# Kernel tuning notes

Measured on AMD Instinct MI355X. Metric: run time of the kernel, lower is better.

Reference implementation:

```python
import jax, jax.numpy as jnp
import numpy as np
from jax import lax

B, N = 4, 32768          # clouds, points per cloud (offsets are equal-sized)
CIN, COUT, S = 128, 256, 2048  # in_channels, out_channels, num_samples
EPS = 1e-5               # BatchNorm eps


def fps(xyz, npoint=S):
    """Farthest point sampling over xyz [N,3]; deterministic start index 0.
    Mirrors the torch loop: record current farthest, update min-distance, argmax."""
    n = xyz.shape[0]

    def step(carry, _):
        distance, farthest = carry
        centroid = xyz[farthest]                       # [3]
        dist = jnp.sum((xyz - centroid) ** 2, axis=1)  # [N]
        distance = jnp.minimum(distance, dist)
        new_farthest = jnp.argmax(distance).astype(jnp.int32)
        return (distance, new_farthest), farthest

    init = (jnp.full((n,), 1e10, dtype=xyz.dtype), jnp.int32(0))
    _, centroids = lax.scan(step, init, None, length=npoint)
    return centroids  # [npoint] int32


def setup_inputs():
    key = jax.random.key(0)
    k1, k2, k3 = jax.random.split(key, 3)
    coord = jax.random.normal(k1, (B * N, 3), dtype=jnp.float32)
    feat = jax.random.normal(k2, (B * N, CIN), dtype=jnp.float32)
    offset = (jnp.arange(1, B + 1, dtype=jnp.int32)) * N  # cumulative counts
    W = jax.random.normal(k3, (COUT, CIN), dtype=jnp.float32) / np.sqrt(CIN)
    gamma = jnp.ones((COUT,), dtype=jnp.float32)
    beta = jnp.zeros((COUT,), dtype=jnp.float32)
    return {"coord": coord, "feat": feat, "offset": offset,
            "W": W, "gamma": gamma, "beta": beta}


def reference(coord, feat, offset, W, gamma, beta):
    # fc -> PointBatchNorm (training-mode batch stats over B*N rows) -> ReLU
    x = feat @ W.T                                  # [B*N, COUT]
    mean = jnp.mean(x, axis=0)
    var = jnp.mean((x - mean) ** 2, axis=0)         # biased var, as torch BN
    x = (x - mean) * lax.rsqrt(var + EPS) * gamma + beta
    x = jax.nn.relu(x)

    coord_b = coord.reshape(B, N, 3)
    feat_b = x.reshape(B, N, COUT)
    idx = jax.vmap(fps)(coord_b)                    # [B, S] int32

    new_coords = jnp.take_along_axis(coord_b, idx[..., None], axis=1).reshape(B * S, 3)
    new_feats = jnp.take_along_axis(feat_b, idx[..., None], axis=1).reshape(B * S, COUT)
    new_offsets = jnp.arange(1, B + 1, dtype=jnp.int32) * S
    return new_coords, new_feats, new_offsets
```

## Files before the change

### kernel.cpp

```cpp
#include <hip/hip_runtime.h>

#define NB 4
#define NPT 32768
#define HPT 16384
#define CIN 128
#define COUT 256
#define NS 2048
#define THR 512
#define PPT 32
#define NG 8

#define WS_G 0
#define WS_FSUM 16384
#define WS_SLOT 16512
#define WS_GSCALE 16544
#define WS_GBIAS 16800
#define WS_IDX 17056

#define OUT_COORD 0
#define OUT_FEAT 24576
#define OUT_OFFS 2121728

__global__ __launch_bounds__(THR) void fused1(
    const float* __restrict__ coord, const float* __restrict__ feat,
    float* __restrict__ wsf, int* __restrict__ wsi,
    unsigned long long* __restrict__ slots)
{
  __shared__ float4 ldsd[NG][THR];
  __shared__ int s_widx[2];
  __shared__ int s_gmaxb[2];
  __shared__ int s_bcast;
  __shared__ float s_fs[4][128];

  const int bid = blockIdx.x;
  const int t = threadIdx.x;
  const bool is_fps = (bid < 4) || (bid >= 8 && bid < 12);

  if (is_fps) {
    const int cl = bid & 3;
    const int h = bid >> 3;
    const int gbase = h * HPT;
    const float* xyz = coord + (size_t)cl * NPT * 3;
    int* idx_out = wsi + cl * NS;
    unsigned long long* slot = slots + cl * 4;

    float px[PPT], py[PPT], pz[PPT];
#pragma unroll
    for (int j = 0; j < PPT; ++j) {
      int p = gbase + j * THR + t;
      px[j] = xyz[p * 3 + 0];
      py[j] = xyz[p * 3 + 1];
      pz[j] = xyz[p * 3 + 2];
    }
#pragma unroll
    for (int g = 0; g < NG; ++g)
      ldsd[g][t] = make_float4(1e10f, 1e10f, 1e10f, 1e10f);
    if (t == 0) {
      if (h == 0) idx_out[0] = 0;
      s_widx[0] = s_widx[1] = 0x7fffffff;
      s_gmaxb[0] = s_gmaxb[1] = 0;
    }
    float cx = xyz[0], cy = xyz[1], cz = xyz[2];
    __syncthreads();

    const int lane = t & 63;
    for (int it = 1; it < NS; ++it) {
      const int par = it & 1;
      float mxa = -1.f, mxb = -1.f;
#pragma unroll
      for (int g = 0; g < NG; ++g) {
        float4 d = ldsd[g][t];
        float nd[4];
#pragma unroll
        for (int k = 0; k < 4; ++k) {
          const int j = 4 * g + k;
          float dx = px[j] - cx, dy = py[j] - cy, dz = pz[j] - cz;
          float sx = dx * dx, sy = dy * dy, sz = dz * dz;
          asm volatile("" : "+v"(sx), "+v"(sy), "+v"(sz));
          float dist = (sx + sy) + sz;
          nd[k] = fminf(k == 0 ? d.x : k == 1 ? d.y : k == 2 ? d.z : d.w, dist);
        }
        ldsd[g][t] = make_float4(nd[0], nd[1], nd[2], nd[3]);
        mxa = fmaxf(mxa, fmaxf(nd[0], nd[1]));
        mxb = fmaxf(mxb, fmaxf(nd[2], nd[3]));
      }
      float lmax = fmaxf(mxa, mxb);
      float wm = lmax;
#pragma unroll
      for (int o = 32; o > 0; o >>= 1) wm = fmaxf(wm, __shfl_xor(wm, o, 64));
      if (lane == 0) atomicMax(&s_gmaxb[par], __float_as_int(wm));
      __syncthreads();
      if (t == 0) { s_gmaxb[par ^ 1] = 0; s_widx[par ^ 1] = 0x7fffffff; }
      const float gmax = __int_as_float(s_gmaxb[par]);
      if (lmax == gmax) {
        int best = 0x7fffffff;
#pragma unroll
        for (int g = 0; g < NG; ++g) {
          float4 d = ldsd[g][t];
          if (d.x == gmax) best = min(best, gbase + (4 * g + 0) * THR + t);
          if (d.y == gmax) best = min(best, gbase + (4 * g + 1) * THR + t);
          if (d.z == gmax) best = min(best, gbase + (4 * g + 2) * THR + t);
          if (d.w == gmax) best = min(best, gbase + (4 * g + 3) * THR + t);
        }
        atomicMin(&s_widx[par], best);
      }
      __syncthreads();
      if (t == 0) {
        unsigned long long mine =
            ((unsigned long long)it << 48) |
            ((unsigned long long)(unsigned)s_gmaxb[par] << 15) |
            (unsigned)(32767 - s_widx[par]);
        __hip_atomic_store(&slot[h * 2 + par], mine,
                           __ATOMIC_RELAXED, __HIP_MEMORY_SCOPE_AGENT);
        unsigned long long other;
        do {
          other = __hip_atomic_load(&slot[(1 - h) * 2 + par],
                                    __ATOMIC_RELAXED, __HIP_MEMORY_SCOPE_AGENT);
        } while ((other >> 48) != (unsigned long long)it);
        unsigned long long win = mine > other ? mine : other;
        int widx = 32767 - (int)(win & 0x7fff);
        s_bcast = widx;
        if (h == 0) idx_out[it] = widx;
      }
      __syncthreads();
      const int widx = s_bcast;
      cx = xyz[widx * 3 + 0];
      cy = xyz[widx * 3 + 1];
      cz = xyz[widx * 3 + 2];
    }
  } else {
    const int g = (bid < 8) ? (bid - 4) : (bid - 8);
    if (g < 128) {
      const float* fr = feat + (size_t)g * 1024 * CIN;
      const int ti = (t & 31) * 4;
      const int tj = (t >> 5) * 8;
      float acc[4][8];
#pragma unroll
      for (int a = 0; a < 4; ++a)
#pragma unroll
        for (int b2 = 0; b2 < 8; ++b2) acc[a][b2] = 0.f;
#pragma unroll 4
      for (int r = 0; r < 1024; ++r) {
        const float* rowp = fr + r * CIN;
        float4 a4 = *(const float4*)(rowp + ti);
        float4 b4 = *(const float4*)(rowp + tj);
        float4 b5 = *(const float4*)(rowp + tj + 4);
        float av[4] = {a4.x, a4.y, a4.z, a4.w};
        float bv[8] = {b4.x, b4.y, b4.z, b4.w, b5.x, b5.y, b5.z, b5.w};
#pragma unroll
        for (int a = 0; a < 4; ++a)
#pragma unroll
          for (int b2 = 0; b2 < 8; ++b2) acc[a][b2] += av[a] * bv[b2];
      }
      float* G = wsf + WS_G;
#pragma unroll
      for (int a = 0; a < 4; ++a)
#pragma unroll
        for (int b2 = 0; b2 < 8; ++b2)
          atomicAdd(&G[(ti + a) * CIN + (tj + b2)], acc[a][b2]);
    } else {
      const int fb = g - 128;
      const size_t base = (size_t)fb * 16384;
      const int c = t & 127, rg = t >> 7;
      float s = 0.f;
      for (int r = rg; r < 16384; r += 4)
        s += feat[(base + r) * CIN + c];
      s_fs[rg][c] = s;
      __syncthreads();
      if (t < 128) {
        float v = s_fs[0][t] + s_fs[1][t] + s_fs[2][t] + s_fs[3][t];
        atomicAdd(&wsf[WS_FSUM + t], v);
      }
    }
  }
}

__global__ __launch_bounds__(128) void finalize_k(
    const float* __restrict__ W, const float* __restrict__ gamma,
    const float* __restrict__ beta, float* __restrict__ wsf)
{
  const int c = blockIdx.x, i = threadIdx.x;
  const float* G = wsf + WS_G;
  const float* fsum = wsf + WS_FSUM;
  const float* Gi = G + i * CIN;
  const float* Wc = W + c * CIN;
  float td = 0.f;
#pragma unroll 8
  for (int j = 0; j < CIN; j += 4) {
    float4 g4 = *(const float4*)(Gi + j);
    float4 w4 = *(const float4*)(Wc + j);
    td += g4.x * w4.x + g4.y * w4.y + g4.z * w4.z + g4.w * w4.w;
  }
  const float wci = Wc[i];
  float q = wci * td;
  float m = fsum[i] * wci;
#pragma unroll
  for (int o = 32; o > 0; o >>= 1) {
    q += __shfl_xor(q, o, 64);
    m += __shfl_xor(m, o, 64);
  }
  __shared__ float sq[2], sm[2];
  if ((i & 63) == 0) { sq[i >> 6] = q; sm[i >> 6] = m; }
  __syncthreads();
  if (i == 0) {
    const float inv_m = 1.f / 131072.f;
    float mean = (sm[0] + sm[1]) * inv_m;
    float e2 = (sq[0] + sq[1]) * inv_m;
    float var = e2 - mean * mean;
    float rstd = rsqrtf(var + 1e-5f);
    float gs = gamma[c] * rstd;
    wsf[WS_GSCALE + c] = gs;
    wsf[WS_GBIAS + c] = beta[c] - mean * gs;
  }
}

__global__ __launch_bounds__(256) void gather_k(
    const float* __restrict__ coord, const float* __restrict__ feat,
    const float* __restrict__ W, const float* __restrict__ wsf,
    const int* __restrict__ wsi, float* __restrict__ out)
{
  const int p = blockIdx.x, t = threadIdx.x;
  const int b = p >> 11;
  const int idx = wsi[p];
  const size_t row = (size_t)b * NPT + idx;
  __shared__ float lf[CIN];
  if (t < CIN) lf[t] = feat[row * CIN + t];
  __syncthreads();
  const float* Wc = W + t * CIN;
  float acc = 0.f;
#pragma unroll 8
  for (int k = 0; k < CIN; k += 4) {
    float4 w4 = *(const float4*)(Wc + k);
    acc += lf[k] * w4.x + lf[k + 1] * w4.y + lf[k + 2] * w4.z + lf[k + 3] * w4.w;
  }
  float y = fmaxf(fmaf(acc, wsf[WS_GSCALE + t], wsf[WS_GBIAS + t]), 0.f);
  out[OUT_FEAT + (size_t)p * COUT + t] = y;
  if (t < 3) out[OUT_COORD + p * 3 + t] = coord[row * 3 + t];
  if (p == 0 && t < 4) out[OUT_OFFS + t] = (float)((t + 1) * NS);
}

extern "C" void kernel_launch(void* const* d_in, const int* in_sizes, int n_in,
                              void* d_out, int out_size, void* d_ws, size_t ws_size,
                              hipStream_t stream)
{
  const float* coord = (const float*)d_in[0];
  const float* feat  = (const float*)d_in[1];
  const float* W     = (const float*)d_in[3];
  const float* gamma = (const float*)d_in[4];
  const float* beta  = (const float*)d_in[5];
  float* wsf = (float*)d_ws;
  int* wsi = (int*)(wsf + WS_IDX);
  unsigned long long* slots = (unsigned long long*)(wsf + WS_SLOT);
  float* out = (float*)d_out;

  hipMemsetAsync(d_ws, 0, (WS_SLOT + 32) * sizeof(float), stream);

  fused1<<<144, THR, 0, stream>>>(coord, feat, wsf, wsi, slots);
  finalize_k<<<COUT, 128, 0, stream>>>(W, gamma, beta, wsf);
  gather_k<<<NB * NS, 256, 0, stream>>>(coord, feat, W, wsf, wsi, out);
}
```

Measured before the change: 5.331 ms.

## Split each FPS cloud across four blocks with register distances and packed argmax keys

Each point cloud's farthest-point sampling now runs on four cooperating blocks instead of two, so each thread holds 16 points. The running min-distances stay in registers rather than in LDS. The two-phase max-then-index reduction is replaced by one 64-bit packed (distance, index) key reduced with shuffles and one LDS atomicMax, which removes a barrier and the rescan. The cross-block handshake now polls three peer slots per iteration, which may add global-memory polling latency on the serial 2048-step critical path.

```diff
diff --git a/kernel.cpp b/kernel.cpp
--- a/kernel.cpp
+++ b/kernel.cpp
@@ -2,20 +2,19 @@
 
 #define NB 4
 #define NPT 32768
-#define HPT 16384
+#define QPT 8192
 #define CIN 128
 #define COUT 256
 #define NS 2048
 #define THR 512
-#define PPT 32
-#define NG 8
+#define PPT 16
 
 #define WS_G 0
 #define WS_FSUM 16384
 #define WS_SLOT 16512
-#define WS_GSCALE 16544
-#define WS_GBIAS 16800
-#define WS_IDX 17056
+#define WS_GSCALE 16576
+#define WS_GBIAS 16832
+#define WS_IDX 17088
 
 #define OUT_COORD 0
 #define OUT_FEAT 24576
@@ -26,39 +25,34 @@
     float* __restrict__ wsf, int* __restrict__ wsi,
     unsigned long long* __restrict__ slots)
 {
-  __shared__ float4 ldsd[NG][THR];
-  __shared__ int s_widx[2];
-  __shared__ int s_gmaxb[2];
+  __shared__ unsigned long long s_key[2];
   __shared__ int s_bcast;
   __shared__ float s_fs[4][128];
 
   const int bid = blockIdx.x;
   const int t = threadIdx.x;
-  const bool is_fps = (bid < 4) || (bid >= 8 && bid < 12);
+  const bool is_fps = (bid < 32) && ((bid & 7) < 4);
 
   if (is_fps) {
     const int cl = bid & 3;
     const int h = bid >> 3;
-    const int gbase = h * HPT;
+    const int gbase = h * QPT;
     const float* xyz = coord + (size_t)cl * NPT * 3;
     int* idx_out = wsi + cl * NS;
-    unsigned long long* slot = slots + cl * 4;
-
-    float px[PPT], py[PPT], pz[PPT];
+    unsigned long long* slot = slots + cl * 8;
+
+    float px[PPT], py[PPT], pz[PPT], dv[PPT];
 #pragma unroll
     for (int j = 0; j < PPT; ++j) {
       int p = gbase + j * THR + t;
       px[j] = xyz[p * 3 + 0];
       py[j] = xyz[p * 3 + 1];
       pz[j] = xyz[p * 3 + 2];
-    }
-#pragma unroll
-    for (int g = 0; g < NG; ++g)
-      ldsd[g][t] = make_float4(1e10f, 1e10f, 1e10f, 1e10f);
+      dv[j] = 1e10f;
+    }
     if (t == 0) {
       if (h == 0) idx_out[0] = 0;
-      s_widx[0] = s_widx[1] = 0x7fffffff;
-      s_gmaxb[0] = s_gmaxb[1] = 0;
+      s_key[0] = s_key[1] = 0ull;
     }
     float cx = xyz[0], cy = xyz[1], cz = xyz[2];
     __syncthreads();
@@ -66,59 +60,51 @@
     const int lane = t & 63;
     for (int it = 1; it < NS; ++it) {
       const int par = it & 1;
-      float mxa = -1.f, mxb = -1.f;
-#pragma unroll
-      for (int g = 0; g < NG; ++g) {
-        float4 d = ldsd[g][t];
-        float nd[4];
-#pragma unroll
-        for (int k = 0; k < 4; ++k) {
-          const int j = 4 * g + k;
-          float dx = px[j] - cx, dy = py[j] - cy, dz = pz[j] - cz;
-          float sx = dx * dx, sy = dy * dy, sz = dz * dz;
-          asm volatile("" : "+v"(sx), "+v"(sy), "+v"(sz));
-          float dist = (sx + sy) + sz;
-          nd[k] = fminf(k == 0 ? d.x : k == 1 ? d.y : k == 2 ? d.z : d.w, dist);
-        }
-        ldsd[g][t] = make_float4(nd[0], nd[1], nd[2], nd[3]);
-        mxa = fmaxf(mxa, fmaxf(nd[0], nd[1]));
-        mxb = fmaxf(mxb, fmaxf(nd[2], nd[3]));
-      }
-      float lmax = fmaxf(mxa, mxb);
-      float wm = lmax;
-#pragma unroll
-      for (int o = 32; o > 0; o >>= 1) wm = fmaxf(wm, __shfl_xor(wm, o, 64));
-      if (lane == 0) atomicMax(&s_gmaxb[par], __float_as_int(wm));
-      __syncthreads();
-      if (t == 0) { s_gmaxb[par ^ 1] = 0; s_widx[par ^ 1] = 0x7fffffff; }
-      const float gmax = __int_as_float(s_gmaxb[par]);
-      if (lmax == gmax) {
-        int best = 0x7fffffff;
-#pragma unroll
-        for (int g = 0; g < NG; ++g) {
-          float4 d = ldsd[g][t];
-          if (d.x == gmax) best = min(best, gbase + (4 * g + 0) * THR + t);
-          if (d.y == gmax) best = min(best, gbase + (4 * g + 1) * THR + t);
-          if (d.z == gmax) best = min(best, gbase + (4 * g + 2) * THR + t);
-          if (d.w == gmax) best = min(best, gbase + (4 * g + 3) * THR + t);
-        }
-        atomicMin(&s_widx[par], best);
-      }
+      float bd = -1.f;
+      int bj = 0;
+#pragma unroll
+      for (int j = 0; j < PPT; ++j) {
+        float dx = px[j] - cx, dy = py[j] - cy, dz = pz[j] - cz;
+        float sx = dx * dx, sy = dy * dy, sz = dz * dz;
+        asm volatile("" : "+v"(sx), "+v"(sy), "+v"(sz));
+        float nd = fminf(dv[j], (sx + sy) + sz);
+        dv[j] = nd;
+        if (nd > bd) { bd = nd; bj = j; }
+      }
+      const int gidx = gbase + bj * THR + t;
+      unsigned long long key =
+          ((unsigned long long)(unsigned)__float_as_int(bd) << 15) |
+          (unsigned)(32767 - gidx);
+#pragma unroll
+      for (int o = 32; o > 0; o >>= 1) {
+        unsigned long long ok = __shfl_xor(key, o, 64);
+        key = ok > key ? ok : key;
+      }
+      if (lane == 0) atomicMax(&s_key[par], key);
       __syncthreads();
       if (t == 0) {
+        s_key[par ^ 1] = 0ull;
         unsigned long long mine =
-            ((unsigned long long)it << 48) |
-            ((unsigned long long)(unsigned)s_gmaxb[par] << 15) |
-            (unsigned)(32767 - s_widx[par]);
+            ((unsigned long long)it << 48) | s_key[par];
         __hip_atomic_store(&slot[h * 2 + par], mine,
                            __ATOMIC_RELAXED, __HIP_MEMORY_SCOPE_AGENT);
-        unsigned long long other;
-        do {
-          other = __hip_atomic_load(&slot[(1 - h) * 2 + par],
+        unsigned long long best = mine;
+        unsigned got = 1u << h;
+        while (got != 0xFu) {
+#pragma unroll
+          for (int p = 0; p < 4; ++p) {
+            if (!(got & (1u << p))) {
+              unsigned long long v =
+                  __hip_atomic_load(&slot[p * 2 + par],
                                     __ATOMIC_RELAXED, __HIP_MEMORY_SCOPE_AGENT);
-        } while ((other >> 48) != (unsigned long long)it);
-        unsigned long long win = mine > other ? mine : other;
-        int widx = 32767 - (int)(win & 0x7fff);
+              if ((v >> 48) == (unsigned long long)it) {
+                got |= 1u << p;
+                if (v > best) best = v;
+              }
+            }
+          }
+        }
+        int widx = 32767 - (int)(best & 0x7fff);
         s_bcast = widx;
         if (h == 0) idx_out[it] = widx;
       }
@@ -129,7 +115,7 @@
       cz = xyz[widx * 3 + 2];
     }
   } else {
-    const int g = (bid < 8) ? (bid - 4) : (bid - 8);
+    const int g = (bid < 32) ? ((bid >> 3) * 4 + (bid & 7) - 4) : (bid - 16);
     if (g < 128) {
       const float* fr = feat + (size_t)g * 1024 * CIN;
       const int ti = (t & 31) * 4;
@@ -253,9 +239,9 @@
   unsigned long long* slots = (unsigned long long*)(wsf + WS_SLOT);
   float* out = (float*)d_out;
 
-  hipMemsetAsync(d_ws, 0, (WS_SLOT + 32) * sizeof(float), stream);
-
-  fused1<<<144, THR, 0, stream>>>(coord, feat, wsf, wsi, slots);
+  hipMemsetAsync(d_ws, 0, (WS_SLOT + 64) * sizeof(float), stream);
+
+  fused1<<<152, THR, 0, stream>>>(coord, feat, wsf, wsi, slots);
   finalize_k<<<COUT, 128, 0, stream>>>(W, gamma, beta, wsf);
   gather_k<<<NB * NS, 256, 0, stream>>>(coord, feat, W, wsf, wsi, out);
 }
```

Measured after the change: 5.140 ms. -3.6%, faster.
